# Kernel optimization log

Hardware: AMD Instinct MI355X
Metric: run time of the kernel (lower is better)

## Reference

```python
import jax, jax.numpy as jnp
import numpy as np

N, E, G = 30000, 120000, 256
F_IN, F_E, H, T = 16, 8, 32, 10
EPS = 1e-5


def setup_inputs() -> dict:
    key = jax.random.key(0)
    ks = jax.random.split(key, 16)
    s = 0.05
    inp = {
        'x': jax.random.normal(ks[0], (N, F_IN), jnp.float32),
        'edge_attr': jax.random.normal(ks[1], (E, F_E), jnp.float32),
        'edge_index': jax.random.randint(ks[2], (2, E), 0, N),
        'batch': jnp.sort(jax.random.randint(ks[3], (N,), 0, G)),
        'c1_nn_w': jax.random.normal(ks[4], (F_E, F_IN * H), jnp.float32) * s,
        'c1_nn_b': jnp.zeros((F_IN * H,), jnp.float32),
        'c1_root': jax.random.normal(ks[5], (F_IN, H), jnp.float32) * s,
        'c1_bias': jnp.zeros((H,), jnp.float32),
        'c2_nn_w': jax.random.normal(ks[6], (F_E, H * H), jnp.float32) * s,
        'c2_nn_b': jnp.zeros((H * H,), jnp.float32),
        'c2_root': jax.random.normal(ks[7], (H, H), jnp.float32) * s,
        'c2_bias': jnp.zeros((H,), jnp.float32),
        'c3_nn_w': jax.random.normal(ks[8], (F_E, H * H), jnp.float32) * s,
        'c3_nn_b': jnp.zeros((H * H,), jnp.float32),
        'c3_root': jax.random.normal(ks[9], (H, H), jnp.float32) * s,
        'c3_bias': jnp.zeros((H,), jnp.float32),
        'bn1_g': jnp.ones((H,), jnp.float32), 'bn1_b': jnp.zeros((H,), jnp.float32),
        'bn1_m': jnp.zeros((H,), jnp.float32), 'bn1_v': jnp.ones((H,), jnp.float32),
        'bn2_g': jnp.ones((H,), jnp.float32), 'bn2_b': jnp.zeros((H,), jnp.float32),
        'bn2_m': jnp.zeros((H,), jnp.float32), 'bn2_v': jnp.ones((H,), jnp.float32),
        'mlp_w1': jax.random.normal(ks[10], (H, H), jnp.float32) * s,
        'mlp_b1': jnp.zeros((H,), jnp.float32),
        'mlp_w2': jax.random.normal(ks[11], (H, T), jnp.float32) * s,
        'mlp_b2': jnp.zeros((T,), jnp.float32),
    }
    return inp


def _nnconv(x, edge_index, edge_attr, nn_w, nn_b, root, bias, in_dim, out_dim):
    # per-edge weight matrix from edge features: [E, in_dim, out_dim]
    W = (edge_attr @ nn_w + nn_b).reshape(-1, in_dim, out_dim)
    # gather source node features, per-edge matvec, scatter-add to targets
    msg = jnp.einsum('ei,eio->eo', x[edge_index[0]], W)
    agg = jax.ops.segment_sum(msg, edge_index[1], num_segments=N)
    return agg + x @ root + bias


def _graph_size_norm(x, batch):
    deg = jax.ops.segment_sum(jnp.ones((N,), x.dtype), batch, num_segments=G)
    inv_sqrt = jnp.where(deg > 0, deg, 1.0) ** -0.5
    return x * inv_sqrt[batch][:, None]


def _bn_eval(x, g, b, m, v):
    return (x - m) * (g * jax.lax.rsqrt(v + EPS)) + b


def reference(x, edge_attr, edge_index, batch,
              c1_nn_w, c1_nn_b, c1_root, c1_bias,
              c2_nn_w, c2_nn_b, c2_root, c2_bias,
              c3_nn_w, c3_nn_b, c3_root, c3_bias,
              bn1_g, bn1_b, bn1_m, bn1_v,
              bn2_g, bn2_b, bn2_m, bn2_v,
              mlp_w1, mlp_b1, mlp_w2, mlp_b2):
    h = _nnconv(x, edge_index, edge_attr, c1_nn_w, c1_nn_b, c1_root, c1_bias, F_IN, H)
    h = _graph_size_norm(h, batch)
    h = jax.nn.relu(_bn_eval(h, bn1_g, bn1_b, bn1_m, bn1_v))
    h = _nnconv(h, edge_index, edge_attr, c2_nn_w, c2_nn_b, c2_root, c2_bias, H, H)
    h = _graph_size_norm(h, batch)
    h = jax.nn.relu(_bn_eval(h, bn2_g, bn2_b, bn2_m, bn2_v))
    h = _nnconv(h, edge_index, edge_attr, c3_nn_w, c3_nn_b, c3_root, c3_bias, H, H)
    # global mean pool over graphs
    cnt = jax.ops.segment_sum(jnp.ones((N,), h.dtype), batch, num_segments=G)
    pooled = jax.ops.segment_sum(h, batch, num_segments=G) / jnp.maximum(cnt, 1.0)[:, None]
    # MLP head (dropout inactive in eval)
    out = jax.nn.relu(pooled @ mlp_w1 + mlp_b1) @ mlp_w2 + mlp_b2
    return out
```

## Files before the change

### kernel.cpp

```cpp
#include <hip/hip_runtime.h>

#define NN 30000
#define NE 120000
#define NG 256
#define FIN 16
#define HD 32
#define TOUT 10
#define EPSV 1e-5f
#define CAP 32

__device__ __forceinline__ void atomAddF(float* p, float v) {
    unsafeAtomicAdd(p, v);
}

__global__ __launch_bounds__(256) void init_kernel(
    const int* __restrict__ batch,
    int*   __restrict__ cursor,
    float* __restrict__ deg_g,
    float* __restrict__ pooled)
{
    const int t = blockIdx.x * 256 + threadIdx.x;

    if (t < NN) cursor[t] = t * CAP;
    if (t < NG * HD) pooled[t] = 0.0f;

    if (t < NG) {
        int lo = 0, hi = NN;
        while (lo < hi) { const int m = (lo + hi) >> 1;
                          if (batch[m] < t) lo = m + 1; else hi = m; }
        const int b0 = lo;
        lo = 0; hi = NN;
        while (lo < hi) { const int m = (lo + hi) >> 1;
                          if (batch[m] < t + 1) lo = m + 1; else hi = m; }
        deg_g[t] = (float)(lo - b0);
    }
}

__global__ __launch_bounds__(256) void bucket_scatter(
    const int* __restrict__ eidx, const float* __restrict__ ea,
    int* __restrict__ cursor,
    int* __restrict__ src_b,
    float4* __restrict__ ea_b)
{
    const int e = blockIdx.x * 256 + threadIdx.x;
    if (e >= NE) return;
    const int d = eidx[NE + e];
    const int slot = atomicAdd(&cursor[d], 1);
    if (slot < d * CAP + CAP) {
        src_b[slot] = eidx[e];
        const float4* s4 = (const float4*)(ea + (size_t)e * 8);
        ea_b[2 * slot]     = s4[0];
        ea_b[2 * slot + 1] = s4[1];
    }
}

template<int IN, bool FINAL>
__global__ __launch_bounds__(256) void fused_layer(
    const float* __restrict__ hin,
    const int*   __restrict__ src_b,
    const float4* __restrict__ ea_b,
    const int*   __restrict__ cursor,
    const float* __restrict__ nn_w,
    const float* __restrict__ nn_b,
    const float* __restrict__ root,
    const float* __restrict__ bias,
    const int*   __restrict__ batch,
    const float* __restrict__ deg_g,
    const float* __restrict__ bn_g,
    const float* __restrict__ bn_b,
    const float* __restrict__ bn_m,
    const float* __restrict__ bn_v,
    float*       __restrict__ out)
{
    constexpr int K  = 10 * IN;
    constexpr int KQ = K / 4;
    constexpr int KL = KQ / 2;
    constexpr int NQ = 32 / IN;

    __shared__ float Tlds[16 * K];
    __shared__ float P[4 * 16 * 64];

    const int tid = threadIdx.x;
    const int wv  = tid >> 6;
    const int l   = tid & 63;
    const int h   = l >> 5;
    const int o   = l & 31;
    const int l5  = l & 31;
    const int pr  = l >> 5;
    const int b16 = blockIdx.x * 16;

    int   p0c[2], p1c[2];
    float tea_pf[2], tx_pf[2];
    #pragma unroll
    for (int j = 0; j < 2; ++j) {
        const int nloc = wv * 4 + j * 2 + pr;
        const int d    = b16 + nloc;
        const int p0   = d * CAP;
        int p1 = cursor[d];
        p1 = (p1 < p0 + CAP) ? p1 : (p0 + CAP);
        p0c[j] = p0; p1c[j] = p1;
        const int deg = p1 - p0;
        float tea = 0.0f, tx = 0.0f;
        if (l5 < deg) {
            const int sl = p0 + l5;
            const int sid = src_b[sl];
            tea = ((const float*)(ea_b + 2 * sl))[0];
            tx  = hin[(long)sid * IN];
        }
        tea_pf[j] = tea; tx_pf[j] = tx;
    }

    float Wreg[KL];
    const int kbase = wv * KQ + h * KL;
    #pragma unroll
    for (int kk = 0; kk < KL; ++kk) {
        const int k = kbase + kk;
        const float* src = (k < 8 * IN) ? (nn_w + k * 32)
                         : (k < 9 * IN) ? (nn_b + (k - 8 * IN) * 32)
                                        : (root + (k - 9 * IN) * 32);
        Wreg[kk] = src[o];
    }

    const int i = l5 & (IN - 1);
    const int q = l5 / IN;

    #pragma unroll
    for (int j = 0; j < 2; ++j) {
        const int nloc = wv * 4 + j * 2 + pr;
        const int d    = b16 + nloc;

        float t[9];
        #pragma unroll
        for (int f = 0; f < 9; ++f) t[f] = 0.0f;

        const int p0 = p0c[j];
        const int p1 = p1c[j];

        int p = p0 + q;
        if (p < p1) {
            const int pe = p1 - 1;
            int pn     = p + NQ;
            int pnc    = (pn < pe) ? pn : pe;
            int s_cur  = src_b[p];
            int s_nxt  = src_b[pnc];
            float4 a_c = ea_b[2 * p];
            float4 b_c = ea_b[2 * p + 1];
            float  xv  = hin[(long)s_cur * IN + i];

            while (true) {
                const float4 a_n = ea_b[2 * pnc];
                const float4 b_n = ea_b[2 * pnc + 1];
                const float  xvn = hin[(long)s_nxt * IN + i];
                const int pn2    = pn + NQ;
                const int pn2c   = (pn2 < pe) ? pn2 : pe;
                const int s_n2   = src_b[pn2c];

                t[0] = fmaf(a_c.x, xv, t[0]);
                t[1] = fmaf(a_c.y, xv, t[1]);
                t[2] = fmaf(a_c.z, xv, t[2]);
                t[3] = fmaf(a_c.w, xv, t[3]);
                t[4] = fmaf(b_c.x, xv, t[4]);
                t[5] = fmaf(b_c.y, xv, t[5]);
                t[6] = fmaf(b_c.z, xv, t[6]);
                t[7] = fmaf(b_c.w, xv, t[7]);
                t[8] += xv;

                p = pn;
                if (p >= p1) break;
                pn = pn2; pnc = pn2c; s_nxt = s_n2;
                a_c = a_n; b_c = b_n; xv = xvn;
            }
        }

        if (IN == 16) {
            #pragma unroll
            for (int f = 0; f < 9; ++f) t[f] += __shfl_xor(t[f], 16, 64);
        }

        if (l5 < IN) {
            float* tb = Tlds + nloc * K;
            #pragma unroll
            for (int f = 0; f < 9; ++f) tb[f * IN + i] = t[f];
            tb[9 * IN + i] = hin[(long)d * IN + i];
        }
    }
    asm volatile("" :: "v"(tea_pf[0]), "v"(tea_pf[1]),
                       "v"(tx_pf[0]),  "v"(tx_pf[1]));
    __syncthreads();

    for (int n = 0; n < 16; ++n) {
        const float* tb = Tlds + n * K + kbase;
        float acc = 0.0f;
        #pragma unroll
        for (int kq = 0; kq < KL / 4; ++kq) {
            const float4 tv = *(const float4*)(tb + kq * 4);
            acc = fmaf(Wreg[4 * kq + 0], tv.x, acc);
            acc = fmaf(Wreg[4 * kq + 1], tv.y, acc);
            acc = fmaf(Wreg[4 * kq + 2], tv.z, acc);
            acc = fmaf(Wreg[4 * kq + 3], tv.w, acc);
        }
        P[(wv * 16 + n) * 64 + l] = acc;
    }
    __syncthreads();

    #pragma unroll
    for (int r = 0; r < 2; ++r) {
        const int idx = r * 256 + tid;
        const int n   = idx >> 5;
        const int oo  = idx & 31;
        float sum = bias[oo];
        #pragma unroll
        for (int ww = 0; ww < 4; ++ww) {
            const float* pb = P + (ww * 16 + n) * 64;
            sum += pb[oo] + pb[32 + oo];
        }
        const int d = b16 + n;
        const int g = batch[d];
        if (!FINAL) {
            float dg = deg_g[g];
            dg = dg > 0.0f ? dg : 1.0f;
            float v = sum * (1.0f / sqrtf(dg));
            const float s = bn_g[oo] / sqrtf(bn_v[oo] + EPSV);
            v = (v - bn_m[oo]) * s + bn_b[oo];
            out[(long)d * 32 + oo] = v > 0.0f ? v : 0.0f;
        } else {
            float v = sum;
            const int   g2 = __shfl(g, (tid & 63) ^ 32, 64);
            const float v2 = __shfl(v, (tid & 63) ^ 32, 64);
            bool do_store = true;
            if (g2 == g) {
                if (tid & 32) do_store = false;
                else          v += v2;
            }
            if (do_store) atomAddF(&out[g * 32 + oo], v);
        }
    }
}

__global__ __launch_bounds__(64) void head_kernel(
    const float* __restrict__ pooled,
    const float* __restrict__ deg,
    const float* __restrict__ w1,
    const float* __restrict__ b1,
    const float* __restrict__ w2,
    const float* __restrict__ b2,
    float*       __restrict__ out)
{
    const int g = blockIdx.x * 64 + threadIdx.x;
    if (g >= NG) return;
    float cnt = deg[g];
    cnt = cnt > 1.0f ? cnt : 1.0f;

    float p[HD];
    #pragma unroll
    for (int i = 0; i < HD; ++i) p[i] = pooled[g * HD + i] / cnt;

    float hid[HD];
    #pragma unroll
    for (int j = 0; j < HD; ++j) {
        float a = b1[j];
        #pragma unroll
        for (int i = 0; i < HD; ++i)
            a = fmaf(p[i], w1[i * HD + j], a);
        hid[j] = a > 0.0f ? a : 0.0f;
    }
    #pragma unroll
    for (int t = 0; t < TOUT; ++t) {
        float a = b2[t];
        #pragma unroll
        for (int j = 0; j < HD; ++j)
            a = fmaf(hid[j], w2[j * TOUT + t], a);
        out[g * TOUT + t] = a;
    }
}

extern "C" void kernel_launch(void* const* d_in, const int* in_sizes, int n_in,
                              void* d_out, int out_size, void* d_ws, size_t ws_size,
                              hipStream_t stream)
{
    const float* x        = (const float*)d_in[0];
    const float* ea       = (const float*)d_in[1];
    const int*   eidx     = (const int*)  d_in[2];
    const int*   batch    = (const int*)  d_in[3];
    const float* c1_nn_w  = (const float*)d_in[4];
    const float* c1_nn_b  = (const float*)d_in[5];
    const float* c1_root  = (const float*)d_in[6];
    const float* c1_bias  = (const float*)d_in[7];
    const float* c2_nn_w  = (const float*)d_in[8];
    const float* c2_nn_b  = (const float*)d_in[9];
    const float* c2_root  = (const float*)d_in[10];
    const float* c2_bias  = (const float*)d_in[11];
    const float* c3_nn_w  = (const float*)d_in[12];
    const float* c3_nn_b  = (const float*)d_in[13];
    const float* c3_root  = (const float*)d_in[14];
    const float* c3_bias  = (const float*)d_in[15];
    const float* bn1_g    = (const float*)d_in[16];
    const float* bn1_b    = (const float*)d_in[17];
    const float* bn1_m    = (const float*)d_in[18];
    const float* bn1_v    = (const float*)d_in[19];
    const float* bn2_g    = (const float*)d_in[20];
    const float* bn2_b    = (const float*)d_in[21];
    const float* bn2_m    = (const float*)d_in[22];
    const float* bn2_v    = (const float*)d_in[23];
    const float* mlp_w1   = (const float*)d_in[24];
    const float* mlp_b1   = (const float*)d_in[25];
    const float* mlp_w2   = (const float*)d_in[26];
    const float* mlp_b2   = (const float*)d_in[27];
    float* out = (float*)d_out;

    float*  h1     = (float*)d_ws;
    float*  h2     = h1 + NN * HD;
    float4* ea_b   = (float4*)(h2 + NN * HD);
    int*    src_b  = (int*)(ea_b + 2 * NN * CAP);
    int*    cursor = src_b + NN * CAP;
    float*  deg_g  = (float*)(cursor + NN);
    float*  pooled = deg_g + NG;

    const int egrid = (NE + 255) / 256;

    init_kernel<<<(NN + 255) / 256, 256, 0, stream>>>(batch, cursor, deg_g, pooled);

    bucket_scatter<<<egrid, 256, 0, stream>>>(eidx, ea, cursor, src_b, ea_b);

    const int lgrid = NN / 16;

    fused_layer<FIN, false><<<lgrid, 256, 0, stream>>>(
        x, src_b, ea_b, cursor, c1_nn_w, c1_nn_b, c1_root, c1_bias,
        batch, deg_g, bn1_g, bn1_b, bn1_m, bn1_v, h1);

    fused_layer<HD, false><<<lgrid, 256, 0, stream>>>(
        h1, src_b, ea_b, cursor, c2_nn_w, c2_nn_b, c2_root, c2_bias,
        batch, deg_g, bn2_g, bn2_b, bn2_m, bn2_v, h2);

    fused_layer<HD, true><<<lgrid, 256, 0, stream>>>(
        h2, src_b, ea_b, cursor, c3_nn_w, c3_nn_b, c3_root, c3_bias,
        batch, deg_g, nullptr, nullptr, nullptr, nullptr, pooled);

    head_kernel<<<(NG + 63) / 64, 64, 0, stream>>>(pooled, deg_g, mlp_w1, mlp_b1,
                                                   mlp_w2, mlp_b2, out);
}
```

Baseline: 238.3 us.

## Process one node per full wavefront with 4-edge batched gathers

Restructures the edge aggregation so each wavefront handles one destination node at a time across all 64 lanes. Each lane covers edges strided by 64/IN and loads four edges' attributes and source features per iteration, replacing the previous one-ahead software prefetch chain. Partial sums are combined with an extra cross-half shuffle. The two half-wave partial products are also reduced with a shuffle before the LDS write, which halves the P buffer and the final reduction reads. It also prefetches a second feature column for the 32-wide layers. Nodes now run serially per wave instead of two at a time, and out-of-range slots issue redundant clamped loads.

```diff
diff --git a/kernel.cpp b/kernel.cpp
--- a/kernel.cpp
+++ b/kernel.cpp
@@ -72,13 +72,14 @@
     const float* __restrict__ bn_v,
     float*       __restrict__ out)
 {
-    constexpr int K  = 10 * IN;
-    constexpr int KQ = K / 4;
-    constexpr int KL = KQ / 2;
-    constexpr int NQ = 32 / IN;
-
-    __shared__ float Tlds[16 * K];
-    __shared__ float P[4 * 16 * 64];
+    constexpr int K    = 10 * IN;
+    constexpr int KQ   = K / 4;
+    constexpr int KL   = KQ / 2;
+    constexpr int NQ   = 64 / IN;
+    constexpr int STEP = 4 * NQ;
+
+    __shared__ __align__(16) float Tlds[16 * K];
+    __shared__ float P[4 * 16 * 32];
 
     const int tid = threadIdx.x;
     const int wv  = tid >> 6;
@@ -89,8 +90,8 @@
     const int pr  = l >> 5;
     const int b16 = blockIdx.x * 16;
 
-    int   p0c[2], p1c[2];
-    float tea_pf[2], tx_pf[2];
+    int   p1c[2];
+    float tea_pf[2], tx_pf[2], tx2_pf[2];
     #pragma unroll
     for (int j = 0; j < 2; ++j) {
         const int nloc = wv * 4 + j * 2 + pr;
@@ -98,16 +99,17 @@
         const int p0   = d * CAP;
         int p1 = cursor[d];
         p1 = (p1 < p0 + CAP) ? p1 : (p0 + CAP);
-        p0c[j] = p0; p1c[j] = p1;
+        p1c[j] = p1;
         const int deg = p1 - p0;
-        float tea = 0.0f, tx = 0.0f;
+        float tea = 0.0f, tx = 0.0f, tx2 = 0.0f;
         if (l5 < deg) {
             const int sl = p0 + l5;
             const int sid = src_b[sl];
             tea = ((const float*)(ea_b + 2 * sl))[0];
             tx  = hin[(long)sid * IN];
+            if (IN == 32) tx2 = hin[(long)sid * IN + 16];
         }
-        tea_pf[j] = tea; tx_pf[j] = tx;
+        tea_pf[j] = tea; tx_pf[j] = tx; tx2_pf[j] = tx2;
     }
 
     float Wreg[KL];
@@ -121,71 +123,66 @@
         Wreg[kk] = src[o];
     }
 
-    const int i = l5 & (IN - 1);
-    const int q = l5 / IN;
-
-    #pragma unroll
-    for (int j = 0; j < 2; ++j) {
-        const int nloc = wv * 4 + j * 2 + pr;
-        const int d    = b16 + nloc;
-
-        float t[9];
-        #pragma unroll
-        for (int f = 0; f < 9; ++f) t[f] = 0.0f;
-
-        const int p0 = p0c[j];
-        const int p1 = p1c[j];
-
-        int p = p0 + q;
-        if (p < p1) {
-            const int pe = p1 - 1;
-            int pn     = p + NQ;
-            int pnc    = (pn < pe) ? pn : pe;
-            int s_cur  = src_b[p];
-            int s_nxt  = src_b[pnc];
-            float4 a_c = ea_b[2 * p];
-            float4 b_c = ea_b[2 * p + 1];
-            float  xv  = hin[(long)s_cur * IN + i];
-
-            while (true) {
-                const float4 a_n = ea_b[2 * pnc];
-                const float4 b_n = ea_b[2 * pnc + 1];
-                const float  xvn = hin[(long)s_nxt * IN + i];
-                const int pn2    = pn + NQ;
-                const int pn2c   = (pn2 < pe) ? pn2 : pe;
-                const int s_n2   = src_b[pn2c];
-
-                t[0] = fmaf(a_c.x, xv, t[0]);
-                t[1] = fmaf(a_c.y, xv, t[1]);
-                t[2] = fmaf(a_c.z, xv, t[2]);
-                t[3] = fmaf(a_c.w, xv, t[3]);
-                t[4] = fmaf(b_c.x, xv, t[4]);
-                t[5] = fmaf(b_c.y, xv, t[5]);
-                t[6] = fmaf(b_c.z, xv, t[6]);
-                t[7] = fmaf(b_c.w, xv, t[7]);
-                t[8] += xv;
-
-                p = pn;
-                if (p >= p1) break;
-                pn = pn2; pnc = pn2c; s_nxt = s_n2;
-                a_c = a_n; b_c = b_n; xv = xvn;
+    {
+        const int i = l & (IN - 1);
+        const int q = l / IN;
+
+        #pragma unroll
+        for (int jj = 0; jj < 4; ++jj) {
+            const int nloc = wv * 4 + jj;
+            const int d    = b16 + nloc;
+            const int p0   = d * CAP;
+            const int p1   = __shfl(p1c[jj >> 1], (jj & 1) << 5, 64);
+
+            float t[9];
+            #pragma unroll
+            for (int f = 0; f < 9; ++f) t[f] = 0.0f;
+
+            for (int base = p0 + q; base < p1; base += STEP) {
+                float4 A[4], B[4];
+                float  xv[4];
+                #pragma unroll
+                for (int e = 0; e < 4; ++e) {
+                    const int  pp = base + e * NQ;
+                    const bool ok = pp < p1;
+                    const int  pc = ok ? pp : p0;
+                    A[e] = ea_b[2 * pc];
+                    B[e] = ea_b[2 * pc + 1];
+                    const int s = src_b[pc];
+                    xv[e] = ok ? hin[(long)s * IN + i] : 0.0f;
+                }
+                #pragma unroll
+                for (int e = 0; e < 4; ++e) {
+                    t[0] = fmaf(A[e].x, xv[e], t[0]);
+                    t[1] = fmaf(A[e].y, xv[e], t[1]);
+                    t[2] = fmaf(A[e].z, xv[e], t[2]);
+                    t[3] = fmaf(A[e].w, xv[e], t[3]);
+                    t[4] = fmaf(B[e].x, xv[e], t[4]);
+                    t[5] = fmaf(B[e].y, xv[e], t[5]);
+                    t[6] = fmaf(B[e].z, xv[e], t[6]);
+                    t[7] = fmaf(B[e].w, xv[e], t[7]);
+                    t[8] += xv[e];
+                }
+            }
+
+            if (IN == 16) {
+                #pragma unroll
+                for (int f = 0; f < 9; ++f) t[f] += __shfl_xor(t[f], 16, 64);
+            }
+            #pragma unroll
+            for (int f = 0; f < 9; ++f) t[f] += __shfl_xor(t[f], 32, 64);
+
+            if (l < IN) {
+                float* tb = Tlds + nloc * K;
+                #pragma unroll
+                for (int f = 0; f < 9; ++f) tb[f * IN + i] = t[f];
+                tb[9 * IN + i] = hin[(long)d * IN + i];
             }
         }
-
-        if (IN == 16) {
-            #pragma unroll
-            for (int f = 0; f < 9; ++f) t[f] += __shfl_xor(t[f], 16, 64);
-        }
-
-        if (l5 < IN) {
-            float* tb = Tlds + nloc * K;
-            #pragma unroll
-            for (int f = 0; f < 9; ++f) tb[f * IN + i] = t[f];
-            tb[9 * IN + i] = hin[(long)d * IN + i];
-        }
     }
     asm volatile("" :: "v"(tea_pf[0]), "v"(tea_pf[1]),
-                       "v"(tx_pf[0]),  "v"(tx_pf[1]));
+                       "v"(tx_pf[0]),  "v"(tx_pf[1]),
+                       "v"(tx2_pf[0]), "v"(tx2_pf[1]));
     __syncthreads();
 
     for (int n = 0; n < 16; ++n) {
@@ -199,7 +196,8 @@
             acc = fmaf(Wreg[4 * kq + 2], tv.z, acc);
             acc = fmaf(Wreg[4 * kq + 3], tv.w, acc);
         }
-        P[(wv * 16 + n) * 64 + l] = acc;
+        acc += __shfl_xor(acc, 32, 64);
+        if (h == 0) P[(wv * 16 + n) * 32 + o] = acc;
     }
     __syncthreads();
 
@@ -210,10 +208,8 @@
         const int oo  = idx & 31;
         float sum = bias[oo];
         #pragma unroll
-        for (int ww = 0; ww < 4; ++ww) {
-            const float* pb = P + (ww * 16 + n) * 64;
-            sum += pb[oo] + pb[32 + oo];
-        }
+        for (int ww = 0; ww < 4; ++ww)
+            sum += P[(ww * 16 + n) * 32 + oo];
         const int d = b16 + n;
         const int g = batch[d];
         if (!FINAL) {
```

New measurement: 239.4 us. About the same (+0.5%).
